# Kernel tuning notes

Measured on AMD Instinct MI355X. Metric: run time of the kernel, lower is better.

The kernel has to match this reference:

```python
import jax, jax.numpy as jnp
import numpy as np

B, N, DIM = 4, 8192, 512
HEADS, DHEAD = 8, 64
INNER = HEADS * DHEAD          # 512
M = 256                        # num landmarks
L = N // M                     # tokens per landmark group (n % m == 0 -> no pad)
ITERS = 6                      # Moore-Penrose iterations
KRES = 33                      # residual depthwise conv kernel (along n)
SCALE = DHEAD ** -0.5


def setup_inputs() -> dict:
    key = jax.random.key(0)
    k1, k2, k3, k4 = jax.random.split(key, 4)
    return {
        "x": jax.random.normal(k1, (B, N, DIM), jnp.float32),
        "w_qkv": jax.random.normal(k2, (DIM, 3 * INNER), jnp.float32) * (DIM ** -0.5),
        "w_out": jax.random.normal(k3, (INNER, DIM), jnp.float32) * (INNER ** -0.5),
        "b_out": jnp.zeros((DIM,), jnp.float32),
        "res_kernel": jax.random.normal(k4, (HEADS, 1, KRES, 1), jnp.float32) * 0.05,
    }


def _moore_penrose_pinv(x, iters=ITERS):
    # x: (b, h, m, m)
    abs_x = jnp.abs(x)
    col = abs_x.sum(axis=-1)
    row = abs_x.sum(axis=-2)
    z = jnp.swapaxes(x, -1, -2) / (jnp.max(col) * jnp.max(row))
    I = jnp.eye(x.shape[-1], dtype=x.dtype)
    for _ in range(iters):
        xz = x @ z
        z = 0.25 * z @ (13 * I - xz @ (15 * I - xz @ (7 * I - xz)))
    return z


def reference(x, w_qkv, w_out, b_out, res_kernel):
    b, n, _ = x.shape
    qkv = x @ w_qkv                               # (b, n, 3*inner)
    q, k, v = jnp.split(qkv, 3, axis=-1)
    to_heads = lambda t: t.reshape(b, n, HEADS, DHEAD).transpose(0, 2, 1, 3)  # (b,h,n,d)
    q, k, v = to_heads(q), to_heads(k), to_heads(v)
    q = q * SCALE

    # landmarks: mean over consecutive groups of L tokens -> (b,h,M,d)
    q_l = q.reshape(b, HEADS, M, L, DHEAD).sum(axis=3) / L
    k_l = k.reshape(b, HEADS, M, L, DHEAD).sum(axis=3) / L

    attn1 = jax.nn.softmax(jnp.einsum('bhid,bhjd->bhij', q, k_l), axis=-1)    # (b,h,n,M)
    attn2 = jax.nn.softmax(jnp.einsum('bhid,bhjd->bhij', q_l, k_l), axis=-1)  # (b,h,M,M)
    attn3 = jax.nn.softmax(jnp.einsum('bhid,bhjd->bhij', q_l, k), axis=-1)    # (b,h,M,n)

    out = attn1 @ _moore_penrose_pinv(attn2) @ (attn3 @ v)                    # (b,h,n,d)

    # depthwise residual conv over the sequence axis, per head
    res = jax.lax.conv_general_dilated(
        v, res_kernel, window_strides=(1, 1),
        padding=[(KRES // 2, KRES // 2), (0, 0)],
        dimension_numbers=('NCHW', 'OIHW', 'NCHW'),
        feature_group_count=HEADS)
    out = out + res

    out = out.transpose(0, 2, 1, 3).reshape(b, n, INNER)
    return out @ w_out + b_out
```

## Files before the change

### kernel.cpp

```cpp
#include <hip/hip_runtime.h>
#include <stdint.h>
#include <stddef.h>


typedef __bf16 bf16x8 __attribute__((ext_vector_type(8)));
typedef __bf16 bf16x4 __attribute__((ext_vector_type(4)));
typedef float f32x4 __attribute__((ext_vector_type(4)));

__device__ __forceinline__ f32x4 mfma_bf16(bf16x8 a, bf16x8 b, f32x4 c) {
    return __builtin_amdgcn_mfma_f32_16x16x32_bf16(a, b, c, 0, 0, 0);
}

__device__ __forceinline__ void gload16(const __bf16* g, __bf16* l) {
    __builtin_amdgcn_global_load_lds(
        (const __attribute__((address_space(1))) void*)g,
        (__attribute__((address_space(3))) void*)l, 16, 0, 0);
}

__global__ void k_init_stats(float* stats) { stats[0] = 1.f; stats[1] = 0.f; }

__global__ __launch_bounds__(256) void k_cvt(const float* __restrict__ in,
        __bf16* __restrict__ out) {
    size_t base = ((size_t)blockIdx.x * 256 + threadIdx.x) * 8;
    float4 a = *(const float4*)&in[base];
    float4 b = *(const float4*)&in[base + 4];
    bf16x8 o;
    o[0] = (__bf16)a.x; o[1] = (__bf16)a.y; o[2] = (__bf16)a.z; o[3] = (__bf16)a.w;
    o[4] = (__bf16)b.x; o[5] = (__bf16)b.y; o[6] = (__bf16)b.z; o[7] = (__bf16)b.w;
    *(bf16x8*)&out[base] = o;
}

__global__ __launch_bounds__(256) void k_transpose_f32(const float* __restrict__ in,
        __bf16* __restrict__ out, int R, int C) {
    __shared__ __bf16 tile[64 * 72];
    int r0 = blockIdx.x * 64, c0 = blockIdx.y * 64;
    int tid = threadIdx.x;
    #pragma unroll
    for (int i = 0; i < 16; ++i) {
        int slot = i * 256 + tid;
        int rr = slot >> 6, cc = slot & 63;
        tile[rr * 72 + cc] = (__bf16)in[(size_t)(r0 + rr) * C + c0 + cc];
    }
    __syncthreads();
    #pragma unroll
    for (int i = 0; i < 2; ++i) {
        int slot = i * 256 + tid;
        int cc = slot >> 3, s = slot & 7;
        bf16x8 t;
        #pragma unroll
        for (int j = 0; j < 8; ++j) t[j] = tile[(s * 8 + j) * 72 + cc];
        *(bf16x8*)&out[(size_t)(c0 + cc) * R + r0 + s * 8] = t;
    }
}

__global__ __launch_bounds__(256) void k_transpose_bf(const __bf16* __restrict__ in,
        __bf16* __restrict__ out, int R, int C, long bsi, long bso) {
    __shared__ __bf16 tile[64 * 72];
    in  += (size_t)blockIdx.z * bsi;
    out += (size_t)blockIdx.z * bso;
    int r0 = blockIdx.x * 64, c0 = blockIdx.y * 64;
    int tid = threadIdx.x;
    #pragma unroll
    for (int i = 0; i < 2; ++i) {
        int slot = i * 256 + tid;
        int rr = slot >> 3, s = slot & 7;
        *(bf16x8*)&tile[rr * 72 + s * 8] =
            *(const bf16x8*)&in[(size_t)(r0 + rr) * C + c0 + s * 8];
    }
    __syncthreads();
    #pragma unroll
    for (int i = 0; i < 2; ++i) {
        int slot = i * 256 + tid;
        int cc = slot >> 3, s = slot & 7;
        bf16x8 t;
        #pragma unroll
        for (int j = 0; j < 8; ++j) t[j] = tile[(s * 8 + j) * 72 + cc];
        *(bf16x8*)&out[(size_t)(c0 + cc) * R + r0 + s * 8] = t;
    }
}

template<int MODE>
__global__ __launch_bounds__(256) void k_gemm_big(const __bf16* __restrict__ A,
        const __bf16* __restrict__ Bt, int K,
        __bf16* __restrict__ qp, __bf16* __restrict__ kp, __bf16* __restrict__ vp,
        float* __restrict__ outp, const float* __restrict__ bias) {
    __shared__ __bf16 sA[128 * 64];
    __shared__ __bf16 sB[128 * 64];
    int tid = threadIdx.x;
    int wave = tid >> 6, l = tid & 63, lm = l & 15, lq = l >> 4;
    int wm = wave & 1, wn = wave >> 1;
    int m0 = blockIdx.x * 128, n0 = blockIdx.y * 128;
    int lr = l >> 3, lc8 = l & 7;
    int src_c = (lc8 ^ lr) * 8;
    f32x4 acc[4][4] = {};
    for (int k0 = 0; k0 < K; k0 += 64) {
        #pragma unroll
        for (int i = 0; i < 4; ++i) {
            int g = wave * 4 + i;
            gload16(&A[(size_t)(m0 + g * 8 + lr) * K + k0 + src_c], &sA[g * 512]);
        }
        #pragma unroll
        for (int i = 0; i < 4; ++i) {
            int g = wave * 4 + i;
            gload16(&Bt[(size_t)(n0 + g * 8 + lr) * K + k0 + src_c], &sB[g * 512]);
        }
        __syncthreads();
        #pragma unroll
        for (int ko = 0; ko < 2; ++ko) {
            int ch = (ko << 2) | lq;
            bf16x8 af[4], bfr[4];
            #pragma unroll
            for (int mi = 0; mi < 4; ++mi) {
                int r = wm * 64 + mi * 16 + lm;
                af[mi] = *(bf16x8*)&sA[r * 64 + ((ch ^ (r & 7)) << 3)];
            }
            #pragma unroll
            for (int ni = 0; ni < 4; ++ni) {
                int r = wn * 64 + ni * 16 + lm;
                bfr[ni] = *(bf16x8*)&sB[r * 64 + ((ch ^ (r & 7)) << 3)];
            }
            #pragma unroll
            for (int mi = 0; mi < 4; ++mi)
                #pragma unroll
                for (int ni = 0; ni < 4; ++ni)
                    acc[mi][ni] = mfma_bf16(af[mi], bfr[ni], acc[mi][ni]);
        }
        __syncthreads();
    }
    #pragma unroll
    for (int mi = 0; mi < 4; ++mi)
    #pragma unroll
    for (int ni = 0; ni < 4; ++ni)
    #pragma unroll
    for (int reg = 0; reg < 4; ++reg) {
        int gr = m0 + wm * 64 + mi * 16 + lq * 4 + reg;
        int gc = n0 + wn * 64 + ni * 16 + lm;
        float v = acc[mi][ni][reg];
        if (MODE == 0) {
            int which = gc >> 9, rem = gc & 511;
            int h = rem >> 6, d = rem & 63;
            int b = gr >> 13, tok = gr & 8191;
            size_t dst = ((size_t)((b * 8 + h) * 8192 + tok)) * 64 + d;
            if (which == 0)      qp[dst] = (__bf16)(v * 0.125f);
            else if (which == 1) kp[dst] = (__bf16)v;
            else                 vp[dst] = (__bf16)v;
        } else {
            outp[(size_t)gr * 512 + gc] = v + bias[gc];
        }
    }
}

__global__ __launch_bounds__(256) void k_landmarks(const __bf16* __restrict__ q,
        const __bf16* __restrict__ k, __bf16* __restrict__ ql, __bf16* __restrict__ kl) {
    int idx = blockIdx.x * 256 + threadIdx.x;
    int sel = idx >> 19;
    int rem = idx & 524287;
    int bh = rem >> 14;
    int m  = (rem >> 6) & 255;
    int d  = rem & 63;
    const __bf16* src = sel ? k : q;
    __bf16* dst = sel ? kl : ql;
    const __bf16* p = src + ((size_t)(bh * 8192 + m * 32)) * 64 + d;
    float s = 0.f;
    #pragma unroll
    for (int j = 0; j < 32; ++j) s += (float)p[j * 64];
    dst[(size_t)bh * 16384 + m * 64 + d] = (__bf16)(s * (1.f / 32.f));
}

__global__ __launch_bounds__(256) void k_attn2(const __bf16* __restrict__ ql,
        const __bf16* __restrict__ kl, __bf16* __restrict__ ph, __bf16* __restrict__ pl) {
    int tid = threadIdx.x;
    int wave = tid >> 6, l = tid & 63, lm = l & 15, lq = l >> 4;
    int bh = blockIdx.y;
    int r0 = blockIdx.x * 64 + wave * 16;
    const __bf16* qb = ql + (size_t)bh * 16384;
    const __bf16* kb = kl + (size_t)bh * 16384;
    bf16x8 af[2];
    #pragma unroll
    for (int ko = 0; ko < 2; ++ko)
        af[ko] = *(const bf16x8*)&qb[(size_t)(r0 + lm) * 64 + ko * 32 + lq * 8];
    f32x4 S[16] = {};
    #pragma unroll
    for (int ci = 0; ci < 16; ++ci)
        #pragma unroll
        for (int ko = 0; ko < 2; ++ko) {
            bf16x8 bfr = *(const bf16x8*)&kb[(size_t)(ci * 16 + lm) * 64 + ko * 32 + lq * 8];
            S[ci] = mfma_bf16(af[ko], bfr, S[ci]);
        }
    __bf16* oh = ph + (size_t)bh * 65536;
    __bf16* ol = pl + (size_t)bh * 65536;
    #pragma unroll
    for (int reg = 0; reg < 4; ++reg) {
        float sum = 0.f;
        #pragma unroll
        for (int ci = 0; ci < 16; ++ci) {
            float e = __expf(S[ci][reg]); S[ci][reg] = e; sum += e;
        }
        #pragma unroll
        for (int msk = 1; msk < 16; msk <<= 1) sum += __shfl_xor(sum, msk);
        float inv = 1.f / sum;
        int row = r0 + lq * 4 + reg;
        #pragma unroll
        for (int ci = 0; ci < 16; ++ci) {
            float v = S[ci][reg] * inv;
            __bf16 hh = (__bf16)v;
            oh[(size_t)row * 256 + ci * 16 + lm] = hh;
            ol[(size_t)row * 256 + ci * 16 + lm] = (__bf16)(v - (float)hh);
        }
    }
}

__global__ __launch_bounds__(256) void k_stats(const __bf16* __restrict__ ph,
        const __bf16* __restrict__ pl, float* stats) {
    __shared__ float red[256];
    int tid = threadIdx.x;
    const __bf16* a = ph + (size_t)blockIdx.x * 65536;
    const __bf16* b = pl + (size_t)blockIdx.x * 65536;
    float cs = 0.f;
    for (int r = 0; r < 256; ++r)
        cs += (float)a[r * 256 + tid] + (float)b[r * 256 + tid];
    red[tid] = cs; __syncthreads();
    for (int off = 128; off > 0; off >>= 1) {
        if (tid < off) red[tid] = fmaxf(red[tid], red[tid + off]);
        __syncthreads();
    }
    if (tid == 0) atomicMax((int*)&stats[1], __float_as_int(red[0]));
}

__global__ __launch_bounds__(256) void k_z0(const __bf16* __restrict__ ph,
        const __bf16* __restrict__ pl, const float* __restrict__ stats,
        __bf16* __restrict__ zh, __bf16* __restrict__ zl) {
    int idx = blockIdx.x * 256 + threadIdx.x;
    int bh = idx >> 16, r = (idx >> 8) & 255, c = idx & 255;
    float inv = 1.f / (stats[0] * stats[1]);
    size_t src = ((size_t)bh << 16) + (size_t)c * 256 + r;
    float v = ((float)ph[src] + (float)pl[src]) * inv;
    __bf16 hh = (__bf16)v;
    zh[idx] = hh;
    zl[idx] = (__bf16)(v - (float)hh);
}

__device__ __forceinline__ void pgemm_core(const __bf16* __restrict__ Ah,
        const __bf16* __restrict__ Al, const __bf16* __restrict__ Bth,
        const __bf16* __restrict__ Btl, int m0, int n0,
        __bf16* sAh, __bf16* sAl, __bf16* sBh, __bf16* sBl, f32x4 acc[2][2]) {
    int tid = threadIdx.x;
    int wave = tid >> 6, l = tid & 63, lm = l & 15, lq = l >> 4;
    int wm = wave & 1, wn = wave >> 1;
    int lr = l >> 3, lc8 = l & 7;
    int src_c = (lc8 ^ lr) * 8;
    for (int k0 = 0; k0 < 256; k0 += 64) {
        #pragma unroll
        for (int i = 0; i < 2; ++i) {
            int g = wave * 2 + i;
            size_t ra = (size_t)(m0 + g * 8 + lr) * 256 + k0 + src_c;
            size_t rb = (size_t)(n0 + g * 8 + lr) * 256 + k0 + src_c;
            gload16(&Ah[ra], &sAh[g * 512]);
            gload16(&Al[ra], &sAl[g * 512]);
            gload16(&Bth[rb], &sBh[g * 512]);
            gload16(&Btl[rb], &sBl[g * 512]);
        }
        __syncthreads();
        #pragma unroll
        for (int ko = 0; ko < 2; ++ko) {
            int ch = (ko << 2) | lq;
            bf16x8 ah[2], al2[2], bh2[2], bl2[2];
            #pragma unroll
            for (int mi = 0; mi < 2; ++mi) {
                int r = wm * 32 + mi * 16 + lm;
                int o = r * 64 + ((ch ^ (r & 7)) << 3);
                ah[mi]  = *(bf16x8*)&sAh[o];
                al2[mi] = *(bf16x8*)&sAl[o];
            }
            #pragma unroll
            for (int ni = 0; ni < 2; ++ni) {
                int r = wn * 32 + ni * 16 + lm;
                int o = r * 64 + ((ch ^ (r & 7)) << 3);
                bh2[ni] = *(bf16x8*)&sBh[o];
                bl2[ni] = *(bf16x8*)&sBl[o];
            }
            #pragma unroll
            for (int mi = 0; mi < 2; ++mi)
                #pragma unroll
                for (int ni = 0; ni < 2; ++ni) {
                    acc[mi][ni] = mfma_bf16(ah[mi], bh2[ni], acc[mi][ni]);
                    acc[mi][ni] = mfma_bf16(ah[mi], bl2[ni], acc[mi][ni]);
                    acc[mi][ni] = mfma_bf16(al2[mi], bh2[ni], acc[mi][ni]);
                }
        }
        __syncthreads();
    }
}

__global__ __launch_bounds__(256) void k_pgemm(const __bf16* __restrict__ Ah,
        const __bf16* __restrict__ Al, const __bf16* __restrict__ Bth,
        const __bf16* __restrict__ Btl, const __bf16* __restrict__ Ch,
        const __bf16* __restrict__ Cl, __bf16* __restrict__ OutH,
        __bf16* __restrict__ OutL, float alpha, const float* __restrict__ sPtr,
        float beta, float delta, int outMode, long bStride) {
    __shared__ __bf16 sAh[64 * 64], sAl[64 * 64], sBh[64 * 64], sBl[64 * 64];
    int tid = threadIdx.x;
    int wave = tid >> 6, l = tid & 63, lm = l & 15, lq = l >> 4;
    int wm = wave & 1, wn = wave >> 1;
    int bh = blockIdx.z;
    int m0 = blockIdx.x * 64, n0 = blockIdx.y * 64;
    float aEff = alpha;
    if (sPtr) aEff *= 1.f / (sPtr[0] * sPtr[1]);
    f32x4 acc[2][2] = {};
    pgemm_core(Ah + (size_t)bh * 65536, Al + (size_t)bh * 65536,
               Bth + (size_t)bh * bStride, Btl + (size_t)bh * bStride,
               m0, n0, sAh, sAl, sBh, sBl, acc);
    #pragma unroll
    for (int mi = 0; mi < 2; ++mi)
    #pragma unroll
    for (int ni = 0; ni < 2; ++ni)
    #pragma unroll
    for (int reg = 0; reg < 4; ++reg) {
        int gr = m0 + wm * 32 + mi * 16 + lq * 4 + reg;
        int gc = n0 + wn * 32 + ni * 16 + lm;
        float v = aEff * acc[mi][ni][reg];
        if (beta != 0.f) {
            size_t ci = (size_t)bh * 65536 + (size_t)gr * 256 + gc;
            v += beta * ((float)Ch[ci] + (float)Cl[ci]);
        }
        if (gr == gc) v += delta;
        if (outMode == 0) {
            size_t di = (size_t)bh * 65536 + (size_t)gr * 256 + gc;
            __bf16 hh = (__bf16)v;
            OutH[di] = hh;
            OutL[di] = (__bf16)(v - (float)hh);
        } else {
            int ci2 = gr >> 4, lqm = (gr >> 2) & 3, r = gr & 3;
            int slot = ((ci2 >> 1) << 5) + (lqm << 3) + ((ci2 & 1) << 2) + r;
            OutH[(size_t)bh * 16384 + (size_t)gc * 256 + slot] = (__bf16)v;
        }
    }
}

__global__ __launch_bounds__(256) void k_pgemm_dual(const __bf16* __restrict__ Zh,
        const __bf16* __restrict__ Zl, const __bf16* __restrict__ A2h,
        const __bf16* __restrict__ A2l, const __bf16* __restrict__ Bth,
        const __bf16* __restrict__ Btl, __bf16* __restrict__ OzH,
        __bf16* __restrict__ OzL, __bf16* __restrict__ OaH, __bf16* __restrict__ OaL) {
    __shared__ __bf16 sAh[64 * 64], sAl[64 * 64], sBh[64 * 64], sBl[64 * 64];
    int tid = threadIdx.x;
    int wave = tid >> 6, l = tid & 63, lm = l & 15, lq = l >> 4;
    int wm = wave & 1, wn = wave >> 1;
    int zz = blockIdx.z, bh = zz & 31;
    const __bf16* Lh = (zz >= 32 ? A2h : Zh) + (size_t)bh * 65536;
    const __bf16* Ll = (zz >= 32 ? A2l : Zl) + (size_t)bh * 65536;
    __bf16* Oh = (zz >= 32 ? OaH : OzH) + (size_t)bh * 65536;
    __bf16* Ol = (zz >= 32 ? OaL : OzL) + (size_t)bh * 65536;
    int m0 = blockIdx.x * 64, n0 = blockIdx.y * 64;
    f32x4 acc[2][2] = {};
    pgemm_core(Lh, Ll, Bth + (size_t)bh * 65536, Btl + (size_t)bh * 65536,
               m0, n0, sAh, sAl, sBh, sBl, acc);
    #pragma unroll
    for (int mi = 0; mi < 2; ++mi)
    #pragma unroll
    for (int ni = 0; ni < 2; ++ni)
    #pragma unroll
    for (int reg = 0; reg < 4; ++reg) {
        int gr = m0 + wm * 32 + mi * 16 + lq * 4 + reg;
        int gc = n0 + wn * 32 + ni * 16 + lm;
        float v = 0.25f * acc[mi][ni][reg];
        __bf16 hh = (__bf16)v;
        Oh[(size_t)gr * 256 + gc] = hh;
        Ol[(size_t)gr * 256 + gc] = (__bf16)(v - (float)hh);
    }
}

__global__ __launch_bounds__(256) void k_attn3(const __bf16* __restrict__ ql,
        const __bf16* __restrict__ kk, const __bf16* __restrict__ vt,
        float* __restrict__ O_s, float* __restrict__ l_s) {
    int tid = threadIdx.x;
    int wave = tid >> 6, l = tid & 63, lm = l & 15, lq = l >> 4;
    int s = blockIdx.x, bh = blockIdx.y;
    const __bf16* qb = ql + (size_t)bh * 16384;
    bf16x8 qa[4][2];
    #pragma unroll
    for (int mi = 0; mi < 4; ++mi)
        #pragma unroll
        for (int ko = 0; ko < 2; ++ko)
            qa[mi][ko] = *(const bf16x8*)&qb[(size_t)(wave * 64 + mi * 16 + lm) * 64 + ko * 32 + lq * 8];
    f32x4 O[4][4] = {};
    float lsum[4] = {};
    for (int it = 0; it < 8; ++it) {
        int c0 = s * 512 + it * 64;
        bf16x8 kf[4][2];
        #pragma unroll
        for (int ci = 0; ci < 4; ++ci)
            #pragma unroll
            for (int ko = 0; ko < 2; ++ko)
                kf[ci][ko] = *(const bf16x8*)&kk[((size_t)bh * 8192 + c0 + ci * 16 + lm) * 64 + ko * 32 + lq * 8];
        f32x4 St[4][4] = {};
        #pragma unroll
        for (int ci = 0; ci < 4; ++ci)
            #pragma unroll
            for (int ko = 0; ko < 2; ++ko)
                #pragma unroll
                for (int mi = 0; mi < 4; ++mi)
                    St[mi][ci] = mfma_bf16(kf[ci][ko], qa[mi][ko], St[mi][ci]);
        bf16x4 pk[4][4];
        #pragma unroll
        for (int mi = 0; mi < 4; ++mi)
            #pragma unroll
            for (int ci = 0; ci < 4; ++ci)
                #pragma unroll
                for (int reg = 0; reg < 4; ++reg) {
                    float e = __expf(St[mi][ci][reg]);
                    lsum[mi] += e;
                    pk[mi][ci][reg] = (__bf16)e;
                }
        #pragma unroll
        for (int ko = 0; ko < 2; ++ko) {
            bf16x8 af[4];
            #pragma unroll
            for (int mi = 0; mi < 4; ++mi)
                #pragma unroll
                for (int r = 0; r < 4; ++r) {
                    af[mi][r]     = pk[mi][2 * ko][r];
                    af[mi][4 + r] = pk[mi][2 * ko + 1][r];
                }
            #pragma unroll
            for (int ni = 0; ni < 4; ++ni) {
                const __bf16* vrow = &vt[((size_t)bh * 64 + ni * 16 + lm) * 8192 + c0 + ko * 32 + lq * 4];
                bf16x4 v0 = *(const bf16x4*)&vrow[0];
                bf16x4 v1 = *(const bf16x4*)&vrow[16];
                bf16x8 vb;
                #pragma unroll
                for (int r = 0; r < 4; ++r) { vb[r] = v0[r]; vb[4 + r] = v1[r]; }
                #pragma unroll
                for (int mi = 0; mi < 4; ++mi)
                    O[mi][ni] = mfma_bf16(af[mi], vb, O[mi][ni]);
            }
        }
    }
    #pragma unroll
    for (int mi = 0; mi < 4; ++mi) {
        float v = lsum[mi];
        v += __shfl_xor(v, 16);
        v += __shfl_xor(v, 32);
        lsum[mi] = v;
    }
    int base = (bh * 16 + s) * 256;
    #pragma unroll
    for (int mi = 0; mi < 4; ++mi)
        if (lq == 0) l_s[base + wave * 64 + mi * 16 + lm] = lsum[mi];
    #pragma unroll
    for (int mi = 0; mi < 4; ++mi)
        #pragma unroll
        for (int reg = 0; reg < 4; ++reg) {
            int r = wave * 64 + mi * 16 + lq * 4 + reg;
            #pragma unroll
            for (int ni = 0; ni < 4; ++ni)
                O_s[((size_t)(base + r)) * 64 + ni * 16 + lm] = O[mi][ni][reg];
        }
}

__global__ __launch_bounds__(256) void k_t2combine(const float* __restrict__ O_s,
        const float* __restrict__ l_s, __bf16* __restrict__ t2th,
        __bf16* __restrict__ t2tl) {
    int idx = blockIdx.x * 256 + threadIdx.x;
    int bh = idx >> 14, r = (idx >> 6) & 255, d = idx & 63;
    float den = 0.f, num = 0.f;
    #pragma unroll
    for (int s = 0; s < 16; ++s) {
        int b2 = (bh * 16 + s) * 256 + r;
        den += l_s[b2];
        num += O_s[(size_t)b2 * 64 + d];
    }
    float v = num / den;
    __bf16 hh = (__bf16)v;
    size_t di = ((size_t)bh * 64 + d) * 256 + r;
    t2th[di] = hh;
    t2tl[di] = (__bf16)(v - (float)hh);
}

__global__ __launch_bounds__(256) void k_conv(const __bf16* __restrict__ vt,
        const float* __restrict__ resk, __bf16* __restrict__ convb) {
    int bh = blockIdx.y, h = bh & 7;
    int d = threadIdx.x & 63, tg = threadIdx.x >> 6;
    int t0 = blockIdx.x * 64 + tg * 16;
    __shared__ float kfs[33];
    if (threadIdx.x < 33) kfs[threadIdx.x] = resk[h * 33 + threadIdx.x];
    __syncthreads();
    const __bf16* row = vt + ((size_t)bh * 64 + d) * 8192;
    float win[48];
    #pragma unroll
    for (int c = 0; c < 6; ++c) {
        int tok0 = t0 - 16 + c * 8;
        if (tok0 >= 0 && tok0 + 7 < 8192) {
            bf16x8 v8 = *(const bf16x8*)&row[tok0];
            #pragma unroll
            for (int e = 0; e < 8; ++e) win[c * 8 + e] = (float)v8[e];
        } else {
            #pragma unroll
            for (int e = 0; e < 8; ++e) {
                int tok = tok0 + e;
                win[c * 8 + e] = (tok >= 0 && tok < 8192) ? (float)row[tok] : 0.f;
            }
        }
    }
    float o[16];
    #pragma unroll
    for (int i = 0; i < 16; ++i) o[i] = 0.f;
    #pragma unroll
    for (int j = 0; j < 33; ++j) {
        float kf = kfs[j];
        #pragma unroll
        for (int i = 0; i < 16; ++i) o[i] += kf * win[i + j];
    }
    __bf16* outr = convb + ((size_t)bh * 8192) * 64 + d;
    #pragma unroll
    for (int i = 0; i < 16; ++i)
        outr[(size_t)(t0 + i) * 64] = (__bf16)o[i];
}

__global__ __launch_bounds__(256) void k_attn1(const __bf16* __restrict__ q,
        const __bf16* __restrict__ kl, const __bf16* __restrict__ zt2p,
        const __bf16* __restrict__ convb, __bf16* __restrict__ outp) {
    int tid = threadIdx.x;
    int wave = tid >> 6, l = tid & 63, lm = l & 15, lq = l >> 4;
    int bh = blockIdx.y;
    int t0 = blockIdx.x * 256;
    int b = bh >> 3, h = bh & 7;
    const __bf16* qb = q + (size_t)bh * 8192 * 64;
    const __bf16* kb = kl + (size_t)bh * 16384;
    const __bf16* zb = zt2p + (size_t)bh * 16384;
    int rowb = t0 + wave * 64;
    bf16x8 qa[4][2];
    #pragma unroll
    for (int mi = 0; mi < 4; ++mi)
        #pragma unroll
        for (int ko = 0; ko < 2; ++ko)
            qa[mi][ko] = *(const bf16x8*)&qb[(size_t)(rowb + mi * 16 + lm) * 64 + ko * 32 + lq * 8];
    f32x4 O[4][4] = {};
    float rs[4] = {};
    #pragma unroll
    for (int c2 = 0; c2 < 8; ++c2) {
        bf16x8 kf[2][2];
        #pragma unroll
        for (int ci = 0; ci < 2; ++ci)
            #pragma unroll
            for (int ko = 0; ko < 2; ++ko)
                kf[ci][ko] = *(const bf16x8*)&kb[(size_t)((c2 * 2 + ci) * 16 + lm) * 64 + ko * 32 + lq * 8];
        f32x4 St[4][2] = {};
        #pragma unroll
        for (int ci = 0; ci < 2; ++ci)
            #pragma unroll
            for (int ko = 0; ko < 2; ++ko)
                #pragma unroll
                for (int mi = 0; mi < 4; ++mi)
                    St[mi][ci] = mfma_bf16(kf[ci][ko], qa[mi][ko], St[mi][ci]);
        bf16x4 pk[4][2];
        #pragma unroll
        for (int mi = 0; mi < 4; ++mi)
            #pragma unroll
            for (int ci = 0; ci < 2; ++ci)
                #pragma unroll
                for (int reg = 0; reg < 4; ++reg) {
                    float e = __expf(St[mi][ci][reg]);
                    rs[mi] += e;
                    pk[mi][ci][reg] = (__bf16)e;
                }
        bf16x8 zfr[4];
        #pragma unroll
        for (int ni = 0; ni < 4; ++ni)
            zfr[ni] = *(const bf16x8*)&zb[(size_t)(ni * 16 + lm) * 256 + c2 * 32 + lq * 8];
        #pragma unroll
        for (int mi = 0; mi < 4; ++mi) {
            bf16x8 af;
            #pragma unroll
            for (int r = 0; r < 4; ++r) {
                af[r]     = pk[mi][0][r];
                af[4 + r] = pk[mi][1][r];
            }
            #pragma unroll
            for (int ni = 0; ni < 4; ++ni)
                O[mi][ni] = mfma_bf16(af, zfr[ni], O[mi][ni]);
        }
    }
    #pragma unroll
    for (int mi = 0; mi < 4; ++mi) {
        float v = rs[mi];
        v += __shfl_xor(v, 16);
        v += __shfl_xor(v, 32);
        float invr[4];
        #pragma unroll
        for (int reg = 0; reg < 4; ++reg)
            invr[reg] = 1.f / __shfl(v, lq * 4 + reg);
        #pragma unroll
        for (int ni = 0; ni < 4; ++ni)
            #pragma unroll
            for (int reg = 0; reg < 4; ++reg) {
                int tok = rowb + mi * 16 + lq * 4 + reg;
                int d = ni * 16 + lm;
                float conv = (float)convb[((size_t)bh * 8192 + tok) * 64 + d];
                float val = O[mi][ni][reg] * invr[reg] + conv;
                outp[((size_t)(b * 8192 + tok)) * 512 + h * 64 + d] = (__bf16)val;
            }
    }
}

extern "C" void kernel_launch(void* const* d_in, const int* in_sizes, int n_in,
                              void* d_out, int out_size, void* d_ws, size_t ws_size,
                              hipStream_t stream) {
    const float* x    = (const float*)d_in[0];
    const float* wqkv = (const float*)d_in[1];
    const float* wout = (const float*)d_in[2];
    const float* bout = (const float*)d_in[3];
    const float* resk = (const float*)d_in[4];
    char* ws = (char*)d_ws;
    size_t off = 0;
    auto alloc = [&](size_t bytes) {
        char* p = ws + off;
        off += (bytes + 255) & ~(size_t)255;
        return p;
    };
    const size_t PL = 2097152;
    __bf16* q_bf   = (__bf16*)alloc(33554432);
    __bf16* k_bf   = (__bf16*)alloc(33554432);
    __bf16* vt     = (__bf16*)alloc(33554432);
    __bf16* outpre = (__bf16*)alloc(33554432);
    __bf16* q_l    = (__bf16*)alloc(1048576);
    __bf16* k_l    = (__bf16*)alloc(1048576);
    __bf16* a2h    = (__bf16*)alloc(8388608);
    __bf16* zAh    = (__bf16*)alloc(8388608);
    __bf16* zBh    = (__bf16*)alloc(8388608);
    __bf16* Amh    = (__bf16*)alloc(8388608);
    __bf16* W2h    = (__bf16*)alloc(8388608);
    __bf16* W3h    = (__bf16*)alloc(8388608);
    float*  O_s    = (float*)alloc(33554432);
    float*  l_s    = (float*)alloc(524288);
    __bf16* t2th   = (__bf16*)alloc(2097152);
    __bf16* zt2t   = (__bf16*)alloc(1048576);
    __bf16* wqkvt  = (__bf16*)alloc(1572864);
    __bf16* woutt  = (__bf16*)alloc(524288);
    float*  stats  = (float*)alloc(256);
    __bf16* convb  = (__bf16*)O_s;
    __bf16* xb     = (__bf16*)O_s;
    __bf16* a2l = a2h + PL;
    __bf16* zAl = zAh + PL;
    __bf16* zBl = zBh + PL;
    __bf16* Aml = Amh + PL;
    __bf16* W2l = W2h + PL;
    __bf16* W3l = W3h + PL;
    __bf16* t2tl = t2th + 524288;

    k_init_stats<<<1, 1, 0, stream>>>(stats);
    k_cvt<<<8192, 256, 0, stream>>>(x, xb);
    k_transpose_f32<<<dim3(8, 24), 256, 0, stream>>>(wqkv, wqkvt, 512, 1536);
    k_transpose_f32<<<dim3(8, 8), 256, 0, stream>>>(wout, woutt, 512, 512);
    k_gemm_big<0><<<dim3(256, 12), 256, 0, stream>>>(xb, wqkvt, 512,
            q_bf, k_bf, outpre, nullptr, nullptr);
    k_transpose_bf<<<dim3(128, 1, 32), 256, 0, stream>>>(outpre, vt, 8192, 64, 524288, 524288);
    k_landmarks<<<4096, 256, 0, stream>>>(q_bf, k_bf, q_l, k_l);
    k_attn2<<<dim3(4, 32), 256, 0, stream>>>(q_l, k_l, a2h, a2l);
    k_stats<<<32, 256, 0, stream>>>(a2h, a2l, stats);
    k_z0<<<8192, 256, 0, stream>>>(a2h, a2l, stats, zAh, zAl);
    k_attn3<<<dim3(16, 32), 256, 0, stream>>>(q_l, k_bf, vt, O_s, l_s);
    k_t2combine<<<2048, 256, 0, stream>>>(O_s, l_s, t2th, t2tl);
    k_conv<<<dim3(128, 32), 256, 0, stream>>>(vt, resk, convb);
    k_pgemm<<<dim3(4, 4, 32), 256, 0, stream>>>(a2h, a2l, a2h, a2l,
            nullptr, nullptr, Amh, Aml, 1.f, stats, 0.f, 0.f, 0, 65536);
    __bf16 *zch = zAh, *zcl = zAl, *znh = zBh, *znl = zBl;
    __bf16 *Ach = Amh, *Acl = Aml, *Anh = a2h, *Anl = a2l;
    for (int it = 0; it < 6; ++it) {
        k_pgemm<<<dim3(4, 4, 32), 256, 0, stream>>>(Ach, Acl, Ach, Acl,
                Ach, Acl, W2h, W2l, 1.f, nullptr, -7.f, 15.f, 0, 65536);
        k_pgemm<<<dim3(4, 4, 32), 256, 0, stream>>>(Ach, Acl, W2h, W2l,
                nullptr, nullptr, W3h, W3l, -1.f, nullptr, 0.f, 13.f, 0, 65536);
        if (it < 5) {
            k_pgemm_dual<<<dim3(4, 4, 64), 256, 0, stream>>>(zch, zcl, Ach, Acl,
                    W3h, W3l, znh, znl, Anh, Anl);
            __bf16* t;
            t = Ach; Ach = Anh; Anh = t;
            t = Acl; Acl = Anl; Anl = t;
        } else {
            k_pgemm_dual<<<dim3(4, 4, 32), 256, 0, stream>>>(zch, zcl, zch, zcl,
                    W3h, W3l, znh, znl, znh, znl);
        }
        __bf16* t;
        t = zch; zch = znh; znh = t;
        t = zcl; zcl = znl; znl = t;
    }
    k_pgemm<<<dim3(4, 1, 32), 256, 0, stream>>>(zch, zcl, t2th, t2tl,
            nullptr, nullptr, zt2t, nullptr, 1.f, nullptr, 0.f, 0.f, 1, 16384);
    k_attn1<<<dim3(32, 32), 256, 0, stream>>>(q_bf, k_l, zt2t, convb, outpre);
    k_gemm_big<1><<<dim3(256, 4), 256, 0, stream>>>(outpre, woutt, 512,
            nullptr, nullptr, nullptr, (float*)d_out, bout);
}
```

Baseline: 696.1 us.

## Fuse Moore-Penrose GEMM chain into one persistent kernel with per-head barriers

Replaces about 20 separate pgemm launches for the pseudo-inverse iterations and the final z@t2 product with a single persistent kernel of 512 blocks. Each head's 16 tiles synchronise through atomic-counter barriers in global memory, which are zeroed by the init kernel. This removes kernel launch gaps and tail drain between dependent small GEMMs. It relies on all 512 blocks being co-resident (launch_bounds 256,2), otherwise the spin barriers can deadlock, and the z and A updates now run sequentially within a block instead of as a 64-slice grid.

```diff
diff --git a/kernel.cpp b/kernel.cpp
--- a/kernel.cpp
+++ b/kernel.cpp
@@ -17,7 +17,11 @@
         (__attribute__((address_space(3))) void*)l, 16, 0, 0);
 }
 
-__global__ void k_init_stats(float* stats) { stats[0] = 1.f; stats[1] = 0.f; }
+__global__ __launch_bounds__(256) void k_init_stats(float* stats, unsigned int* bars) {
+    int idx = blockIdx.x * 256 + threadIdx.x;
+    if (idx == 0) { stats[0] = 1.f; stats[1] = 0.f; }
+    if (idx < 1024) bars[idx] = 0u;
+}
 
 __global__ __launch_bounds__(256) void k_cvt(const float* __restrict__ in,
         __bf16* __restrict__ out) {
@@ -292,20 +296,18 @@
     }
 }
 
-__global__ __launch_bounds__(256) void k_pgemm(const __bf16* __restrict__ Ah,
+__device__ __forceinline__ void pstage(const __bf16* __restrict__ Ah,
         const __bf16* __restrict__ Al, const __bf16* __restrict__ Bth,
         const __bf16* __restrict__ Btl, const __bf16* __restrict__ Ch,
         const __bf16* __restrict__ Cl, __bf16* __restrict__ OutH,
-        __bf16* __restrict__ OutL, float alpha, const float* __restrict__ sPtr,
-        float beta, float delta, int outMode, long bStride) {
-    __shared__ __bf16 sAh[64 * 64], sAl[64 * 64], sBh[64 * 64], sBl[64 * 64];
+        __bf16* __restrict__ OutL, float alpha, float beta, float delta,
+        int outMode, long bStride, int bid,
+        __bf16* sAh, __bf16* sAl, __bf16* sBh, __bf16* sBl) {
     int tid = threadIdx.x;
     int wave = tid >> 6, l = tid & 63, lm = l & 15, lq = l >> 4;
     int wm = wave & 1, wn = wave >> 1;
-    int bh = blockIdx.z;
-    int m0 = blockIdx.x * 64, n0 = blockIdx.y * 64;
-    float aEff = alpha;
-    if (sPtr) aEff *= 1.f / (sPtr[0] * sPtr[1]);
+    int bh = bid >> 4;
+    int m0 = (bid & 3) * 64, n0 = ((bid >> 2) & 3) * 64;
     f32x4 acc[2][2] = {};
     pgemm_core(Ah + (size_t)bh * 65536, Al + (size_t)bh * 65536,
                Bth + (size_t)bh * bStride, Btl + (size_t)bh * bStride,
@@ -318,7 +320,7 @@
     for (int reg = 0; reg < 4; ++reg) {
         int gr = m0 + wm * 32 + mi * 16 + lq * 4 + reg;
         int gc = n0 + wn * 32 + ni * 16 + lm;
-        float v = aEff * acc[mi][ni][reg];
+        float v = alpha * acc[mi][ni][reg];
         if (beta != 0.f) {
             size_t ci = (size_t)bh * 65536 + (size_t)gr * 256 + gc;
             v += beta * ((float)Ch[ci] + (float)Cl[ci]);
@@ -337,37 +339,67 @@
     }
 }
 
-__global__ __launch_bounds__(256) void k_pgemm_dual(const __bf16* __restrict__ Zh,
-        const __bf16* __restrict__ Zl, const __bf16* __restrict__ A2h,
-        const __bf16* __restrict__ A2l, const __bf16* __restrict__ Bth,
-        const __bf16* __restrict__ Btl, __bf16* __restrict__ OzH,
-        __bf16* __restrict__ OzL, __bf16* __restrict__ OaH, __bf16* __restrict__ OaL) {
+__global__ __launch_bounds__(256, 2) void k_pchain(
+        __bf16* a2h, __bf16* a2l, __bf16* zAh, __bf16* zAl,
+        __bf16* zBh, __bf16* zBl, __bf16* Amh, __bf16* Aml,
+        __bf16* W2h, __bf16* W2l, __bf16* W3h, __bf16* W3l,
+        __bf16* t2th, __bf16* t2tl, __bf16* zt2t, const float* stats,
+        unsigned int* bars) {
     __shared__ __bf16 sAh[64 * 64], sAl[64 * 64], sBh[64 * 64], sBl[64 * 64];
-    int tid = threadIdx.x;
-    int wave = tid >> 6, l = tid & 63, lm = l & 15, lq = l >> 4;
-    int wm = wave & 1, wn = wave >> 1;
-    int zz = blockIdx.z, bh = zz & 31;
-    const __bf16* Lh = (zz >= 32 ? A2h : Zh) + (size_t)bh * 65536;
-    const __bf16* Ll = (zz >= 32 ? A2l : Zl) + (size_t)bh * 65536;
-    __bf16* Oh = (zz >= 32 ? OaH : OzH) + (size_t)bh * 65536;
-    __bf16* Ol = (zz >= 32 ? OaL : OzL) + (size_t)bh * 65536;
-    int m0 = blockIdx.x * 64, n0 = blockIdx.y * 64;
-    f32x4 acc[2][2] = {};
-    pgemm_core(Lh, Ll, Bth + (size_t)bh * 65536, Btl + (size_t)bh * 65536,
-               m0, n0, sAh, sAl, sBh, sBl, acc);
-    #pragma unroll
-    for (int mi = 0; mi < 2; ++mi)
-    #pragma unroll
-    for (int ni = 0; ni < 2; ++ni)
-    #pragma unroll
-    for (int reg = 0; reg < 4; ++reg) {
-        int gr = m0 + wm * 32 + mi * 16 + lq * 4 + reg;
-        int gc = n0 + wn * 32 + ni * 16 + lm;
-        float v = 0.25f * acc[mi][ni][reg];
-        __bf16 hh = (__bf16)v;
-        Oh[(size_t)gr * 256 + gc] = hh;
-        Ol[(size_t)gr * 256 + gc] = (__bf16)(v - (float)hh);
-    }
+    int b = blockIdx.x;
+    int c = b & 7, j = b >> 3;
+    int bh = c * 4 + (j >> 4);
+    int t16 = j & 15;
+    int bid = t16 | (bh << 4);
+    unsigned int* cnt = bars + bh * 32;
+    unsigned int target = 0;
+
+    auto bar = [&]() {
+        __syncthreads();
+        target += 16;
+        if (threadIdx.x == 0) {
+            __threadfence();
+            atomicAdd(cnt, 1u);
+            while (atomicAdd(cnt, 0u) < target)
+                __builtin_amdgcn_s_sleep(2);
+            __threadfence();
+        }
+        __syncthreads();
+    };
+
+    float sc = 1.f / (stats[0] * stats[1]);
+    pstage(a2h, a2l, a2h, a2l, nullptr, nullptr, Amh, Aml,
+           sc, 0.f, 0.f, 0, 65536, bid, sAh, sAl, sBh, sBl);
+    bar();
+    __bf16 *zch = zAh, *zcl = zAl, *znh = zBh, *znl = zBl;
+    __bf16 *Ach = Amh, *Acl = Aml, *Anh = a2h, *Anl = a2l;
+    for (int it = 0; it < 6; ++it) {
+        pstage(Ach, Acl, Ach, Acl, Ach, Acl, W2h, W2l,
+               1.f, -7.f, 15.f, 0, 65536, bid, sAh, sAl, sBh, sBl);
+        bar();
+        pstage(Ach, Acl, W2h, W2l, nullptr, nullptr, W3h, W3l,
+               -1.f, 0.f, 13.f, 0, 65536, bid, sAh, sAl, sBh, sBl);
+        bar();
+        if (it < 5) {
+            pstage(zch, zcl, W3h, W3l, nullptr, nullptr, znh, znl,
+                   0.25f, 0.f, 0.f, 0, 65536, bid, sAh, sAl, sBh, sBl);
+            pstage(Ach, Acl, W3h, W3l, nullptr, nullptr, Anh, Anl,
+                   0.25f, 0.f, 0.f, 0, 65536, bid, sAh, sAl, sBh, sBl);
+            __bf16* t;
+            t = Ach; Ach = Anh; Anh = t;
+            t = Acl; Acl = Anl; Anl = t;
+        } else {
+            pstage(zch, zcl, W3h, W3l, nullptr, nullptr, znh, znl,
+                   0.25f, 0.f, 0.f, 0, 65536, bid, sAh, sAl, sBh, sBl);
+        }
+        bar();
+        __bf16* t;
+        t = zch; zch = znh; znh = t;
+        t = zcl; zcl = znl; znl = t;
+    }
+    if (t16 < 4)
+        pstage(zch, zcl, t2th, t2tl, nullptr, nullptr, zt2t, nullptr,
+               1.f, 0.f, 0.f, 1, 16384, t16 | (bh << 4), sAh, sAl, sBh, sBl);
 }
 
 __global__ __launch_bounds__(256) void k_attn3(const __bf16* __restrict__ ql,
@@ -638,6 +670,7 @@
     __bf16* wqkvt  = (__bf16*)alloc(1572864);
     __bf16* woutt  = (__bf16*)alloc(524288);
     float*  stats  = (float*)alloc(256);
+    unsigned int* bars = (unsigned int*)alloc(4096);
     __bf16* convb  = (__bf16*)O_s;
     __bf16* xb     = (__bf16*)O_s;
     __bf16* a2l = a2h + PL;
@@ -648,7 +681,7 @@
     __bf16* W3l = W3h + PL;
     __bf16* t2tl = t2th + 524288;
 
-    k_init_stats<<<1, 1, 0, stream>>>(stats);
+    k_init_stats<<<4, 256, 0, stream>>>(stats, bars);
     k_cvt<<<8192, 256, 0, stream>>>(x, xb);
     k_transpose_f32<<<dim3(8, 24), 256, 0, stream>>>(wqkv, wqkvt, 512, 1536);
     k_transpose_f32<<<dim3(8, 8), 256, 0, stream>>>(wout, woutt, 512, 512);
@@ -662,31 +695,10 @@
     k_attn3<<<dim3(16, 32), 256, 0, stream>>>(q_l, k_bf, vt, O_s, l_s);
     k_t2combine<<<2048, 256, 0, stream>>>(O_s, l_s, t2th, t2tl);
     k_conv<<<dim3(128, 32), 256, 0, stream>>>(vt, resk, convb);
-    k_pgemm<<<dim3(4, 4, 32), 256, 0, stream>>>(a2h, a2l, a2h, a2l,
-            nullptr, nullptr, Amh, Aml, 1.f, stats, 0.f, 0.f, 0, 65536);
-    __bf16 *zch = zAh, *zcl = zAl, *znh = zBh, *znl = zBl;
-    __bf16 *Ach = Amh, *Acl = Aml, *Anh = a2h, *Anl = a2l;
-    for (int it = 0; it < 6; ++it) {
-        k_pgemm<<<dim3(4, 4, 32), 256, 0, stream>>>(Ach, Acl, Ach, Acl,
-                Ach, Acl, W2h, W2l, 1.f, nullptr, -7.f, 15.f, 0, 65536);
-        k_pgemm<<<dim3(4, 4, 32), 256, 0, stream>>>(Ach, Acl, W2h, W2l,
-                nullptr, nullptr, W3h, W3l, -1.f, nullptr, 0.f, 13.f, 0, 65536);
-        if (it < 5) {
-            k_pgemm_dual<<<dim3(4, 4, 64), 256, 0, stream>>>(zch, zcl, Ach, Acl,
-                    W3h, W3l, znh, znl, Anh, Anl);
-            __bf16* t;
-            t = Ach; Ach = Anh; Anh = t;
-            t = Acl; Acl = Anl; Anl = t;
-        } else {
-            k_pgemm_dual<<<dim3(4, 4, 32), 256, 0, stream>>>(zch, zcl, zch, zcl,
-                    W3h, W3l, znh, znl, znh, znl);
-        }
-        __bf16* t;
-        t = zch; zch = znh; znh = t;
-        t = zcl; zcl = znl; znl = t;
-    }
-    k_pgemm<<<dim3(4, 1, 32), 256, 0, stream>>>(zch, zcl, t2th, t2tl,
-            nullptr, nullptr, zt2t, nullptr, 1.f, nullptr, 0.f, 0.f, 1, 16384);
+
+    k_pchain<<<512, 256, 0, stream>>>(a2h, a2l, zAh, zAl, zBh, zBl,
+            Amh, Aml, W2h, W2l, W3h, W3l, t2th, t2tl, zt2t, stats, bars);
+
     k_attn1<<<dim3(32, 32), 256, 0, stream>>>(q_bf, k_l, zt2t, convb, outpre);
     k_gemm_big<1><<<dim3(256, 4), 256, 0, stream>>>(outpre, woutt, 512,
             nullptr, nullptr, nullptr, (float*)d_out, bout);
```

New measurement: 1.253 ms. 80.1% more time.
